# Optimization experiments

Measured on AMD Instinct MI355X. Metric: run time of the kernel, lower is better.

The kernel has to match this reference:

```python
import jax, jax.numpy as jnp
import numpy as np

B, N, L, ND = 512, 4096, 128, 1


def setup_inputs() -> dict:
    key = jax.random.key(0)
    ks = jax.random.split(key, 20)
    g = lambda k, shape, s=0.05: jax.random.normal(k, shape, dtype=jnp.float32) * s
    IN = 3 * L + ND  # MLP input: [mem, mem, delta_t, x]
    inp = {
        "x": jax.random.normal(ks[0], (B, N, ND), jnp.float32),
        "memory": jax.random.normal(ks[1], (N, L), jnp.float32),
        "delta_t": jax.random.normal(ks[2], (B, N, L), jnp.float32),
        "src_w1": g(ks[3], (L, IN)), "src_b1": g(ks[4], (L,)),
        "src_w2": g(ks[5], (L, L)), "src_b2": g(ks[6], (L,)),
        "tar_w1": g(ks[7], (L, IN)), "tar_b1": g(ks[8], (L,)),
        "tar_w2": g(ks[9], (L, L)), "tar_b2": g(ks[10], (L,)),
        "gru_wih": g(ks[11], (3 * L, L)), "gru_whh": g(ks[12], (3 * L, L)),
        "gru_bih": g(ks[13], (3 * L,)), "gru_bhh": g(ks[14], (3 * L,)),
        "source": jax.random.randint(ks[15], (B, 1), 0, N, dtype=jnp.int64),
        "target": jax.random.randint(ks[16], (B, 1), 0, N, dtype=jnp.int64),
    }
    return inp


def _mlp(h, w1, b1, w2, b2):
    return jax.nn.relu(h @ w1.T + b1) @ w2.T + b2


def _gru_cell(inp, h, wih, whh, bih, bhh):
    gi = inp @ wih.T + bih          # [n, 3L]
    gh = h @ whh.T + bhh            # [n, 3L]
    i_r, i_z, i_n = jnp.split(gi, 3, axis=-1)
    h_r, h_z, h_n = jnp.split(gh, 3, axis=-1)
    r = jax.nn.sigmoid(i_r + h_r)
    z = jax.nn.sigmoid(i_z + h_z)
    n = jnp.tanh(i_n + r * h_n)
    return (1.0 - z) * n + z * h


def reference(x, memory, delta_t, src_w1, src_b1, src_w2, src_b2,
              tar_w1, tar_b1, tar_w2, tar_b2,
              gru_wih, gru_whh, gru_bih, gru_bhh, source, target):
    b = x.shape[0]
    bi = jnp.arange(b)
    s = source[:, 0]
    t = target[:, 0]
    src_mem = memory[s]                 # [B, L]
    tar_mem = memory[t]                 # [B, L]
    src_x = x[bi, s, :]                 # [B, ND]
    tar_x = x[bi, t, :]
    src_dt = delta_t[bi, s, :]          # [B, L]
    tar_dt = delta_t[bi, t, :]
    src_in = jnp.concatenate([src_mem, tar_mem, src_dt, src_x], axis=-1)
    tar_in = jnp.concatenate([tar_mem, src_mem, tar_dt, tar_x], axis=-1)
    src_msg = _mlp(src_in, src_w1, src_b1, src_w2, src_b2)
    tar_msg = _mlp(tar_in, tar_w1, tar_b1, tar_w2, tar_b2)

    # unique + scatter_mean == segment-mean over node ids, touching only seen nodes
    ids = jnp.concatenate([s, t], axis=0)                       # [2B]
    msgs = jnp.concatenate([src_msg, tar_msg], axis=0)          # [2B, L]
    n_nodes = memory.shape[0]
    msg_sum = jax.ops.segment_sum(msgs, ids, num_segments=n_nodes)
    cnt = jax.ops.segment_sum(jnp.ones((ids.shape[0],), msgs.dtype), ids,
                              num_segments=n_nodes)
    agg = msg_sum / jnp.maximum(cnt, 1.0)[:, None]              # [N, L]
    new_mem = _gru_cell(agg, memory, gru_wih, gru_whh, gru_bih, gru_bhh)
    seen = (cnt > 0)[:, None]
    return jnp.where(seen, new_mem, memory)
```

## Files before the change

kernel.cpp:

```cpp
#include <hip/hip_runtime.h>
#include <math.h>

#define BB 512
#define NN 4096
#define LL 128
#define IN_DIM 385
#define IN_PAD 388
#define NK4_1 97
#define NK4_2 32
#define EPB 2
#define GPB 4

#define OFF_MSG   0
#define OFF_CNT   (OFF_MSG + NN * LL)
#define OFF_COUNT (OFF_CNT + NN)
#define OFF_LIST  (OFF_COUNT + 4)
#define OFF_W1PS  529416
#define OFF_W1PT  (OFF_W1PS + NK4_1 * LL * 4)
#define OFF_W2PS  (OFF_W1PT + NK4_1 * LL * 4)
#define OFF_W2PT  (OFF_W2PS + NK4_2 * LL * 4)
#define OFF_WIHP  (OFF_W2PT + NK4_2 * LL * 4)
#define OFF_WHHP  (OFF_WIHP + 3 * NK4_2 * LL * 4)

__global__ __launch_bounds__(256) void prep_kernel(
    const float* __restrict__ sw1, const float* __restrict__ tw1,
    const float* __restrict__ sw2, const float* __restrict__ tw2,
    const float* __restrict__ wih, const float* __restrict__ whh,
    float* __restrict__ ws)
{
    const int i = blockIdx.x * 256 + threadIdx.x;
    const int stride = gridDim.x * 256;

    float4* msg4 = (float4*)(ws + OFF_MSG);
    const float4 z4 = make_float4(0.f, 0.f, 0.f, 0.f);
    for (int idx = i; idx < NN * LL / 4; idx += stride)
        msg4[idx] = z4;
    for (int idx = i; idx < NN; idx += stride)
        ws[OFF_CNT + idx] = 0.0f;
    if (i == 0)
        ((int*)ws)[OFF_COUNT] = 0;

    float4* w1ps = (float4*)(ws + OFF_W1PS);
    float4* w1pt = (float4*)(ws + OFF_W1PT);
    for (int idx = i; idx < NK4_1 * LL; idx += stride) {
        const int k4 = idx >> 7, j = idx & 127;
        const int k = k4 * 4;
        float4 a, b;
        a.x = sw1[j * IN_DIM + k];     b.x = tw1[j * IN_DIM + k];
        a.y = (k + 1 < IN_DIM) ? sw1[j * IN_DIM + k + 1] : 0.f;
        b.y = (k + 1 < IN_DIM) ? tw1[j * IN_DIM + k + 1] : 0.f;
        a.z = (k + 2 < IN_DIM) ? sw1[j * IN_DIM + k + 2] : 0.f;
        b.z = (k + 2 < IN_DIM) ? tw1[j * IN_DIM + k + 2] : 0.f;
        a.w = (k + 3 < IN_DIM) ? sw1[j * IN_DIM + k + 3] : 0.f;
        b.w = (k + 3 < IN_DIM) ? tw1[j * IN_DIM + k + 3] : 0.f;
        w1ps[idx] = a; w1pt[idx] = b;
    }
    float4* w2ps = (float4*)(ws + OFF_W2PS);
    float4* w2pt = (float4*)(ws + OFF_W2PT);
    for (int idx = i; idx < NK4_2 * LL; idx += stride) {
        const int k4 = idx >> 7, j = idx & 127;
        const int k = k4 * 4;
        w2ps[idx] = make_float4(sw2[j * LL + k], sw2[j * LL + k + 1],
                                sw2[j * LL + k + 2], sw2[j * LL + k + 3]);
        w2pt[idx] = make_float4(tw2[j * LL + k], tw2[j * LL + k + 1],
                                tw2[j * LL + k + 2], tw2[j * LL + k + 3]);
    }
    float4* wihp = (float4*)(ws + OFF_WIHP);
    float4* whhp = (float4*)(ws + OFF_WHHP);
    for (int idx = i; idx < 3 * NK4_2 * LL; idx += stride) {
        const int j = idx & 127;
        const int gk = idx >> 7;
        const int gate = gk >> 5, k4 = gk & 31;
        const int row = gate * LL + j, k = k4 * 4;
        wihp[idx] = make_float4(wih[row * LL + k], wih[row * LL + k + 1],
                                wih[row * LL + k + 2], wih[row * LL + k + 3]);
        whhp[idx] = make_float4(whh[row * LL + k], whh[row * LL + k + 1],
                                whh[row * LL + k + 2], whh[row * LL + k + 3]);
    }
}

__global__ __launch_bounds__(256) void edge_msg_kernel(
    const float* __restrict__ x,
    const float* __restrict__ memory,
    const float* __restrict__ delta_t,
    const float* __restrict__ sb1, const float* __restrict__ sb2,
    const float* __restrict__ tb1, const float* __restrict__ tb2,
    const int* __restrict__ source, const int* __restrict__ target,
    float* __restrict__ ws, float* __restrict__ out)
{
    const int tid = threadIdx.x;

    if (blockIdx.x >= 512) {
        const int cb = blockIdx.x - 512;
        float4* out4 = (float4*)out;
        const float4* mem4 = (const float4*)memory;
        for (int idx = cb * 256 + tid; idx < NN * LL / 4; idx += 32 * 256)
            out4[idx] = mem4[idx];
        return;
    }

    const int side  = blockIdx.x & 1;
    const int chunk = blockIdx.x >> 1;
    const int g     = tid >> 7;
    const int j     = tid & 127;

    __shared__ float in2[IN_PAD][EPB];
    __shared__ float h1[LL][EPB];
    __shared__ float part1[2][EPB][LL];
    __shared__ float part2[2][EPB][LL];
    __shared__ int   node_sh[EPB];

    const float4* w1p = (const float4*)(ws + (side ? OFF_W1PT : OFF_W1PS));
    const float4* w2p = (const float4*)(ws + (side ? OFF_W2PT : OFF_W2PS));
    const float* b1  = side ? tb1 : sb1;
    const float* b2  = side ? tb2 : sb2;

    #pragma unroll
    for (int e = 0; e < EPB; ++e) {
        const int eg = chunk * EPB + e;
        const int s = source[eg], t = target[eg];
        const int node  = side ? t : s;
        const int other = side ? s : t;
        if (tid == 0) node_sh[e] = node;
        for (int idx = tid; idx < IN_PAD; idx += 256) {
            float v = 0.0f;
            if (idx < LL)           v = memory[node * LL + idx];
            else if (idx < 2 * LL)  v = memory[other * LL + (idx - LL)];
            else if (idx < 3 * LL)  v = delta_t[((size_t)eg * NN + node) * LL + (idx - 2 * LL)];
            else if (idx == 3 * LL) v = x[(size_t)eg * NN + node];
            in2[idx][e] = v;
        }
    }
    __syncthreads();

    {
        const int k40 = g ? 49 : 0;
        const int k41 = g ? NK4_1 : 49;
        float a0 = 0.f, a1 = 0.f;
        #pragma unroll 4
        for (int k4 = k40; k4 < k41; ++k4) {
            const float4 w  = w1p[k4 * LL + j];
            const float4 i0 = *(const float4*)&in2[k4 * 4][0];
            const float4 i1 = *(const float4*)&in2[k4 * 4 + 2][0];
            a0 = fmaf(w.x, i0.x, a0); a1 = fmaf(w.x, i0.y, a1);
            a0 = fmaf(w.y, i0.z, a0); a1 = fmaf(w.y, i0.w, a1);
            a0 = fmaf(w.z, i1.x, a0); a1 = fmaf(w.z, i1.y, a1);
            a0 = fmaf(w.w, i1.z, a0); a1 = fmaf(w.w, i1.w, a1);
        }
        part1[g][0][j] = a0;
        part1[g][1][j] = a1;
    }
    __syncthreads();

    h1[j][g] = fmaxf(part1[0][g][j] + part1[1][g][j] + b1[j], 0.0f);
    __syncthreads();

    {
        const int k40 = g * 16, k41 = k40 + 16;
        float a0 = 0.f, a1 = 0.f;
        #pragma unroll 4
        for (int k4 = k40; k4 < k41; ++k4) {
            const float4 w  = w2p[k4 * LL + j];
            const float4 h0 = *(const float4*)&h1[k4 * 4][0];
            const float4 h2 = *(const float4*)&h1[k4 * 4 + 2][0];
            a0 = fmaf(w.x, h0.x, a0); a1 = fmaf(w.x, h0.y, a1);
            a0 = fmaf(w.y, h0.z, a0); a1 = fmaf(w.y, h0.w, a1);
            a0 = fmaf(w.z, h2.x, a0); a1 = fmaf(w.z, h2.y, a1);
            a0 = fmaf(w.w, h2.z, a0); a1 = fmaf(w.w, h2.w, a1);
        }
        part2[g][0][j] = a0;
        part2[g][1][j] = a1;
    }
    __syncthreads();

    {
        const float m = part2[0][g][j] + part2[1][g][j] + b2[j];
        atomicAdd(ws + OFF_MSG + node_sh[g] * LL + j, m);
    }
    if (tid < EPB) {
        const int node = node_sh[tid];
        const float old = atomicAdd(ws + OFF_CNT + node, 1.0f);
        if (old == 0.0f) {
            const int pos = atomicAdd((int*)ws + OFF_COUNT, 1);
            ((int*)ws)[OFF_LIST + pos] = node;
        }
    }
}

__global__ __launch_bounds__(256) void gru_kernel(
    const float* __restrict__ memory,
    const float* __restrict__ bih, const float* __restrict__ bhh,
    float* __restrict__ ws, float* __restrict__ out)
{
    const int tid = threadIdx.x;
    const int g = tid >> 7, j = tid & 127;
    const int scount = ((const int*)ws)[OFF_COUNT];
    const int base = blockIdx.x * GPB;
    if (base >= scount) return;
    const int nact = min(GPB, scount - base);

    __shared__ float ah[LL][2 * GPB];
    __shared__ float gates[6][GPB][LL];
    __shared__ int   nodes_sh[GPB];

    if (tid < GPB)
        nodes_sh[tid] = (base + tid < scount)
                        ? ((const int*)ws)[OFF_LIST + base + tid] : -1;
    __syncthreads();

    #pragma unroll
    for (int gi = 0; gi < GPB; ++gi) {
        const int node = nodes_sh[gi];
        if (g == 0) {
            float v = 0.0f;
            if (node >= 0) {
                const float c = ws[OFF_CNT + node];
                v = ws[OFF_MSG + node * LL + j] / c;
            }
            ah[j][gi] = v;
        } else {
            ah[j][GPB + gi] = (node >= 0) ? memory[node * LL + j] : 0.0f;
        }
    }
    __syncthreads();

    const float4* wp = (const float4*)(ws + (g ? OFF_WHHP : OFF_WIHP));
    float a0[GPB] = {}, a1[GPB] = {}, a2[GPB] = {};
    #pragma unroll 2
    for (int k4 = 0; k4 < NK4_2; ++k4) {
        const float4 w0 = wp[(0 * NK4_2 + k4) * LL + j];
        const float4 w1 = wp[(1 * NK4_2 + k4) * LL + j];
        const float4 w2 = wp[(2 * NK4_2 + k4) * LL + j];
        const float w0a[4] = {w0.x, w0.y, w0.z, w0.w};
        const float w1a[4] = {w1.x, w1.y, w1.z, w1.w};
        const float w2a[4] = {w2.x, w2.y, w2.z, w2.w};
        #pragma unroll
        for (int c = 0; c < 4; ++c) {
            const float4 v4 = *(const float4*)&ah[k4 * 4 + c][g * GPB];
            const float va[4] = {v4.x, v4.y, v4.z, v4.w};
            #pragma unroll
            for (int gi = 0; gi < GPB; ++gi) {
                a0[gi] = fmaf(w0a[c], va[gi], a0[gi]);
                a1[gi] = fmaf(w1a[c], va[gi], a1[gi]);
                a2[gi] = fmaf(w2a[c], va[gi], a2[gi]);
            }
        }
    }
    #pragma unroll
    for (int gi = 0; gi < GPB; ++gi) {
        gates[g * 3 + 0][gi][j] = a0[gi];
        gates[g * 3 + 1][gi][j] = a1[gi];
        gates[g * 3 + 2][gi][j] = a2[gi];
    }
    __syncthreads();

    const int total = nact * LL;
    for (int o = tid; o < total; o += 256) {
        const int gi = o >> 7, jj = o & 127;
        const int node = nodes_sh[gi];
        const float ir = gates[0][gi][jj] + bih[jj];
        const float iz = gates[1][gi][jj] + bih[LL + jj];
        const float inn = gates[2][gi][jj] + bih[2 * LL + jj];
        const float hr = gates[3][gi][jj] + bhh[jj];
        const float hz = gates[4][gi][jj] + bhh[LL + jj];
        const float hn = gates[5][gi][jj] + bhh[2 * LL + jj];
        const float r = 1.0f / (1.0f + __expf(-(ir + hr)));
        const float z = 1.0f / (1.0f + __expf(-(iz + hz)));
        const float n = tanhf(inn + r * hn);
        const float h = ah[jj][GPB + gi];
        out[node * LL + jj] = (1.0f - z) * n + z * h;
    }
}

extern "C" void kernel_launch(void* const* d_in, const int* in_sizes, int n_in,
                              void* d_out, int out_size, void* d_ws, size_t ws_size,
                              hipStream_t stream) {
    const float* x        = (const float*)d_in[0];
    const float* memory   = (const float*)d_in[1];
    const float* delta_t  = (const float*)d_in[2];
    const float* src_w1   = (const float*)d_in[3];
    const float* src_b1   = (const float*)d_in[4];
    const float* src_w2   = (const float*)d_in[5];
    const float* src_b2   = (const float*)d_in[6];
    const float* tar_w1   = (const float*)d_in[7];
    const float* tar_b1   = (const float*)d_in[8];
    const float* tar_w2   = (const float*)d_in[9];
    const float* tar_b2   = (const float*)d_in[10];
    const float* gru_wih  = (const float*)d_in[11];
    const float* gru_whh  = (const float*)d_in[12];
    const float* gru_bih  = (const float*)d_in[13];
    const float* gru_bhh  = (const float*)d_in[14];
    const int*   source   = (const int*)d_in[15];
    const int*   target   = (const int*)d_in[16];

    float* out = (float*)d_out;
    float* ws  = (float*)d_ws;

    prep_kernel<<<512, 256, 0, stream>>>(
        src_w1, tar_w1, src_w2, tar_w2, gru_wih, gru_whh, ws);

    edge_msg_kernel<<<544, 256, 0, stream>>>(
        x, memory, delta_t, src_b1, src_b2, tar_b1, tar_b2,
        source, target, ws, out);

    gru_kernel<<<1024 / GPB, 256, 0, stream>>>(
        memory, gru_bih, gru_bhh, ws, out);
}
```

Baseline: 37.11 us.

## Read MLP and GRU inputs directly from global memory instead of LDS staging

Both kernels stop staging gathered input rows into shared memory. The message MLP now splits its input by segment (own memory, other memory, delta_t, x) across the two thread groups, and each thread reads wavefront-uniform float4s straight from global memory. The GRU kernel reads the message and memory rows directly and applies the 1/count scale after the matvec, which removes a staging pass and a barrier in each kernel. In exchange every thread issues redundant broadcast global loads that rely on cache hits, and the first layer's work split between the two halves changes slightly.

```diff
diff --git a/kernel.cpp b/kernel.cpp
--- a/kernel.cpp
+++ b/kernel.cpp
@@ -5,7 +5,6 @@
 #define NN 4096
 #define LL 128
 #define IN_DIM 385
-#define IN_PAD 388
 #define NK4_1 97
 #define NK4_2 32
 #define EPB 2
@@ -104,48 +103,78 @@
     const int g     = tid >> 7;
     const int j     = tid & 127;
 
-    __shared__ float in2[IN_PAD][EPB];
+    const int eg0 = chunk * EPB, eg1 = eg0 + 1;
+    const int s0 = source[eg0], t0 = target[eg0];
+    const int s1 = source[eg1], t1 = target[eg1];
+    const int node0  = side ? t0 : s0, other0 = side ? s0 : t0;
+    const int node1  = side ? t1 : s1, other1 = side ? s1 : t1;
+
     __shared__ float h1[LL][EPB];
     __shared__ float part1[2][EPB][LL];
     __shared__ float part2[2][EPB][LL];
-    __shared__ int   node_sh[EPB];
 
     const float4* w1p = (const float4*)(ws + (side ? OFF_W1PT : OFF_W1PS));
     const float4* w2p = (const float4*)(ws + (side ? OFF_W2PT : OFF_W2PS));
     const float* b1  = side ? tb1 : sb1;
     const float* b2  = side ? tb2 : sb2;
 
-    #pragma unroll
-    for (int e = 0; e < EPB; ++e) {
-        const int eg = chunk * EPB + e;
-        const int s = source[eg], t = target[eg];
-        const int node  = side ? t : s;
-        const int other = side ? s : t;
-        if (tid == 0) node_sh[e] = node;
-        for (int idx = tid; idx < IN_PAD; idx += 256) {
-            float v = 0.0f;
-            if (idx < LL)           v = memory[node * LL + idx];
-            else if (idx < 2 * LL)  v = memory[other * LL + (idx - LL)];
-            else if (idx < 3 * LL)  v = delta_t[((size_t)eg * NN + node) * LL + (idx - 2 * LL)];
-            else if (idx == 3 * LL) v = x[(size_t)eg * NN + node];
-            in2[idx][e] = v;
-        }
-    }
-    __syncthreads();
-
     {
-        const int k40 = g ? 49 : 0;
-        const int k41 = g ? NK4_1 : 49;
         float a0 = 0.f, a1 = 0.f;
-        #pragma unroll 4
-        for (int k4 = k40; k4 < k41; ++k4) {
-            const float4 w  = w1p[k4 * LL + j];
-            const float4 i0 = *(const float4*)&in2[k4 * 4][0];
-            const float4 i1 = *(const float4*)&in2[k4 * 4 + 2][0];
-            a0 = fmaf(w.x, i0.x, a0); a1 = fmaf(w.x, i0.y, a1);
-            a0 = fmaf(w.y, i0.z, a0); a1 = fmaf(w.y, i0.w, a1);
-            a0 = fmaf(w.z, i1.x, a0); a1 = fmaf(w.z, i1.y, a1);
-            a0 = fmaf(w.w, i1.z, a0); a1 = fmaf(w.w, i1.w, a1);
+        const float* dA = delta_t + ((size_t)eg0 * NN + node0) * LL;
+        const float* dB = delta_t + ((size_t)eg1 * NN + node1) * LL;
+        if (g == 0) {
+            const float* pA = memory + (size_t)node0 * LL;
+            const float* pB = memory + (size_t)node1 * LL;
+            #pragma unroll 4
+            for (int k4 = 0; k4 < 32; ++k4) {
+                const float4 w  = w1p[k4 * LL + j];
+                const float4 iA = *(const float4*)(pA + 4 * k4);
+                const float4 iB = *(const float4*)(pB + 4 * k4);
+                a0 = fmaf(w.x, iA.x, a0); a1 = fmaf(w.x, iB.x, a1);
+                a0 = fmaf(w.y, iA.y, a0); a1 = fmaf(w.y, iB.y, a1);
+                a0 = fmaf(w.z, iA.z, a0); a1 = fmaf(w.z, iB.z, a1);
+                a0 = fmaf(w.w, iA.w, a0); a1 = fmaf(w.w, iB.w, a1);
+            }
+            #pragma unroll 4
+            for (int k4 = 64; k4 < 80; ++k4) {
+                const float4 w  = w1p[k4 * LL + j];
+                const float4 iA = *(const float4*)(dA + 4 * (k4 - 64));
+                const float4 iB = *(const float4*)(dB + 4 * (k4 - 64));
+                a0 = fmaf(w.x, iA.x, a0); a1 = fmaf(w.x, iB.x, a1);
+                a0 = fmaf(w.y, iA.y, a0); a1 = fmaf(w.y, iB.y, a1);
+                a0 = fmaf(w.z, iA.z, a0); a1 = fmaf(w.z, iB.z, a1);
+                a0 = fmaf(w.w, iA.w, a0); a1 = fmaf(w.w, iB.w, a1);
+            }
+        } else {
+            const float* pA = memory + (size_t)other0 * LL;
+            const float* pB = memory + (size_t)other1 * LL;
+            #pragma unroll 4
+            for (int k4 = 32; k4 < 64; ++k4) {
+                const float4 w  = w1p[k4 * LL + j];
+                const float4 iA = *(const float4*)(pA + 4 * (k4 - 32));
+                const float4 iB = *(const float4*)(pB + 4 * (k4 - 32));
+                a0 = fmaf(w.x, iA.x, a0); a1 = fmaf(w.x, iB.x, a1);
+                a0 = fmaf(w.y, iA.y, a0); a1 = fmaf(w.y, iB.y, a1);
+                a0 = fmaf(w.z, iA.z, a0); a1 = fmaf(w.z, iB.z, a1);
+                a0 = fmaf(w.w, iA.w, a0); a1 = fmaf(w.w, iB.w, a1);
+            }
+            #pragma unroll 4
+            for (int k4 = 80; k4 < 96; ++k4) {
+                const float4 w  = w1p[k4 * LL + j];
+                const float4 iA = *(const float4*)(dA + 4 * (k4 - 64));
+                const float4 iB = *(const float4*)(dB + 4 * (k4 - 64));
+                a0 = fmaf(w.x, iA.x, a0); a1 = fmaf(w.x, iB.x, a1);
+                a0 = fmaf(w.y, iA.y, a0); a1 = fmaf(w.y, iB.y, a1);
+                a0 = fmaf(w.z, iA.z, a0); a1 = fmaf(w.z, iB.z, a1);
+                a0 = fmaf(w.w, iA.w, a0); a1 = fmaf(w.w, iB.w, a1);
+            }
+            {
+                const float4 w = w1p[96 * LL + j];
+                const float xA = x[(size_t)eg0 * NN + node0];
+                const float xB = x[(size_t)eg1 * NN + node1];
+                a0 = fmaf(w.x, xA, a0);
+                a1 = fmaf(w.x, xB, a1);
+            }
         }
         part1[g][0][j] = a0;
         part1[g][1][j] = a1;
@@ -174,11 +203,12 @@
     __syncthreads();
 
     {
+        const int node = g ? node1 : node0;
         const float m = part2[0][g][j] + part2[1][g][j] + b2[j];
-        atomicAdd(ws + OFF_MSG + node_sh[g] * LL + j, m);
+        atomicAdd(ws + OFF_MSG + (size_t)node * LL + j, m);
     }
     if (tid < EPB) {
-        const int node = node_sh[tid];
+        const int node = tid ? node1 : node0;
         const float old = atomicAdd(ws + OFF_CNT + node, 1.0f);
         if (old == 0.0f) {
             const int pos = atomicAdd((int*)ws + OFF_COUNT, 1);
@@ -190,7 +220,8 @@
 __global__ __launch_bounds__(256) void gru_kernel(
     const float* __restrict__ memory,
     const float* __restrict__ bih, const float* __restrict__ bhh,
-    float* __restrict__ ws, float* __restrict__ out)
+    const float* __restrict__ ws,
+    float* __restrict__ out)
 {
     const int tid = threadIdx.x;
     const int g = tid >> 7, j = tid & 127;
@@ -199,30 +230,33 @@
     if (base >= scount) return;
     const int nact = min(GPB, scount - base);
 
-    __shared__ float ah[LL][2 * GPB];
     __shared__ float gates[6][GPB][LL];
     __shared__ int   nodes_sh[GPB];
 
-    if (tid < GPB)
-        nodes_sh[tid] = (base + tid < scount)
-                        ? ((const int*)ws)[OFF_LIST + base + tid] : -1;
-    __syncthreads();
-
+    int nd[GPB];
     #pragma unroll
-    for (int gi = 0; gi < GPB; ++gi) {
-        const int node = nodes_sh[gi];
-        if (g == 0) {
-            float v = 0.0f;
-            if (node >= 0) {
-                const float c = ws[OFF_CNT + node];
-                v = ws[OFF_MSG + node * LL + j] / c;
-            }
-            ah[j][gi] = v;
-        } else {
-            ah[j][GPB + gi] = (node >= 0) ? memory[node * LL + j] : 0.0f;
-        }
-    }
-    __syncthreads();
+    for (int s = 0; s < GPB; ++s)
+        nd[s] = (base + s < scount) ? ((const int*)ws)[OFF_LIST + base + s]
+                                    : ((const int*)ws)[OFF_LIST + base];
+    if (tid < GPB) nodes_sh[tid] = nd[tid];
+
+    const float* op0; const float* op1; const float* op2; const float* op3;
+    float rc0 = 1.f, rc1 = 1.f, rc2 = 1.f, rc3 = 1.f;
+    if (g == 0) {
+        op0 = ws + OFF_MSG + (size_t)nd[0] * LL;
+        op1 = ws + OFF_MSG + (size_t)nd[1] * LL;
+        op2 = ws + OFF_MSG + (size_t)nd[2] * LL;
+        op3 = ws + OFF_MSG + (size_t)nd[3] * LL;
+        rc0 = 1.0f / ws[OFF_CNT + nd[0]];
+        rc1 = 1.0f / ws[OFF_CNT + nd[1]];
+        rc2 = 1.0f / ws[OFF_CNT + nd[2]];
+        rc3 = 1.0f / ws[OFF_CNT + nd[3]];
+    } else {
+        op0 = memory + (size_t)nd[0] * LL;
+        op1 = memory + (size_t)nd[1] * LL;
+        op2 = memory + (size_t)nd[2] * LL;
+        op3 = memory + (size_t)nd[3] * LL;
+    }
 
     const float4* wp = (const float4*)(ws + (g ? OFF_WHHP : OFF_WIHP));
     float a0[GPB] = {}, a1[GPB] = {}, a2[GPB] = {};
@@ -231,44 +265,67 @@
         const float4 w0 = wp[(0 * NK4_2 + k4) * LL + j];
         const float4 w1 = wp[(1 * NK4_2 + k4) * LL + j];
         const float4 w2 = wp[(2 * NK4_2 + k4) * LL + j];
-        const float w0a[4] = {w0.x, w0.y, w0.z, w0.w};
-        const float w1a[4] = {w1.x, w1.y, w1.z, w1.w};
-        const float w2a[4] = {w2.x, w2.y, w2.z, w2.w};
-        #pragma unroll
-        for (int c = 0; c < 4; ++c) {
-            const float4 v4 = *(const float4*)&ah[k4 * 4 + c][g * GPB];
-            const float va[4] = {v4.x, v4.y, v4.z, v4.w};
-            #pragma unroll
-            for (int gi = 0; gi < GPB; ++gi) {
-                a0[gi] = fmaf(w0a[c], va[gi], a0[gi]);
-                a1[gi] = fmaf(w1a[c], va[gi], a1[gi]);
-                a2[gi] = fmaf(w2a[c], va[gi], a2[gi]);
-            }
-        }
+        const float4 v0 = *(const float4*)(op0 + 4 * k4);
+        const float4 v1 = *(const float4*)(op1 + 4 * k4);
+        const float4 v2 = *(const float4*)(op2 + 4 * k4);
+        const float4 v3 = *(const float4*)(op3 + 4 * k4);
+        a0[0] = fmaf(w0.x, v0.x, a0[0]); a0[0] = fmaf(w0.y, v0.y, a0[0]);
+        a0[0] = fmaf(w0.z, v0.z, a0[0]); a0[0] = fmaf(w0.w, v0.w, a0[0]);
+        a1[0] = fmaf(w1.x, v0.x, a1[0]); a1[0] = fmaf(w1.y, v0.y, a1[0]);
+        a1[0] = fmaf(w1.z, v0.z, a1[0]); a1[0] = fmaf(w1.w, v0.w, a1[0]);
+        a2[0] = fmaf(w2.x, v0.x, a2[0]); a2[0] = fmaf(w2.y, v0.y, a2[0]);
+        a2[0] = fmaf(w2.z, v0.z, a2[0]); a2[0] = fmaf(w2.w, v0.w, a2[0]);
+
+        a0[1] = fmaf(w0.x, v1.x, a0[1]); a0[1] = fmaf(w0.y, v1.y, a0[1]);
+        a0[1] = fmaf(w0.z, v1.z, a0[1]); a0[1] = fmaf(w0.w, v1.w, a0[1]);
+        a1[1] = fmaf(w1.x, v1.x, a1[1]); a1[1] = fmaf(w1.y, v1.y, a1[1]);
+        a1[1] = fmaf(w1.z, v1.z, a1[1]); a1[1] = fmaf(w1.w, v1.w, a1[1]);
+        a2[1] = fmaf(w2.x, v1.x, a2[1]); a2[1] = fmaf(w2.y, v1.y, a2[1]);
+        a2[1] = fmaf(w2.z, v1.z, a2[1]); a2[1] = fmaf(w2.w, v1.w, a2[1]);
+
+        a0[2] = fmaf(w0.x, v2.x, a0[2]); a0[2] = fmaf(w0.y, v2.y, a0[2]);
+        a0[2] = fmaf(w0.z, v2.z, a0[2]); a0[2] = fmaf(w0.w, v2.w, a0[2]);
+        a1[2] = fmaf(w1.x, v2.x, a1[2]); a1[2] = fmaf(w1.y, v2.y, a1[2]);
+        a1[2] = fmaf(w1.z, v2.z, a1[2]); a1[2] = fmaf(w1.w, v2.w, a1[2]);
+        a2[2] = fmaf(w2.x, v2.x, a2[2]); a2[2] = fmaf(w2.y, v2.y, a2[2]);
+        a2[2] = fmaf(w2.z, v2.z, a2[2]); a2[2] = fmaf(w2.w, v2.w, a2[2]);
+
+        a0[3] = fmaf(w0.x, v3.x, a0[3]); a0[3] = fmaf(w0.y, v3.y, a0[3]);
+        a0[3] = fmaf(w0.z, v3.z, a0[3]); a0[3] = fmaf(w0.w, v3.w, a0[3]);
+        a1[3] = fmaf(w1.x, v3.x, a1[3]); a1[3] = fmaf(w1.y, v3.y, a1[3]);
+        a1[3] = fmaf(w1.z, v3.z, a1[3]); a1[3] = fmaf(w1.w, v3.w, a1[3]);
+        a2[3] = fmaf(w2.x, v3.x, a2[3]); a2[3] = fmaf(w2.y, v3.y, a2[3]);
+        a2[3] = fmaf(w2.z, v3.z, a2[3]); a2[3] = fmaf(w2.w, v3.w, a2[3]);
+    }
+    if (g == 0) {
+        a0[0] *= rc0; a1[0] *= rc0; a2[0] *= rc0;
+        a0[1] *= rc1; a1[1] *= rc1; a2[1] *= rc1;
+        a0[2] *= rc2; a1[2] *= rc2; a2[2] *= rc2;
+        a0[3] *= rc3; a1[3] *= rc3; a2[3] *= rc3;
     }
     #pragma unroll
-    for (int gi = 0; gi < GPB; ++gi) {
-        gates[g * 3 + 0][gi][j] = a0[gi];
-        gates[g * 3 + 1][gi][j] = a1[gi];
-        gates[g * 3 + 2][gi][j] = a2[gi];
+    for (int s = 0; s < GPB; ++s) {
+        gates[g * 3 + 0][s][j] = a0[s];
+        gates[g * 3 + 1][s][j] = a1[s];
+        gates[g * 3 + 2][s][j] = a2[s];
     }
     __syncthreads();
 
     const int total = nact * LL;
     for (int o = tid; o < total; o += 256) {
-        const int gi = o >> 7, jj = o & 127;
-        const int node = nodes_sh[gi];
-        const float ir = gates[0][gi][jj] + bih[jj];
-        const float iz = gates[1][gi][jj] + bih[LL + jj];
-        const float inn = gates[2][gi][jj] + bih[2 * LL + jj];
-        const float hr = gates[3][gi][jj] + bhh[jj];
-        const float hz = gates[4][gi][jj] + bhh[LL + jj];
-        const float hn = gates[5][gi][jj] + bhh[2 * LL + jj];
+        const int s = o >> 7, jj = o & 127;
+        const int node = nodes_sh[s];
+        const float ir = gates[0][s][jj] + bih[jj];
+        const float iz = gates[1][s][jj] + bih[LL + jj];
+        const float inn = gates[2][s][jj] + bih[2 * LL + jj];
+        const float hr = gates[3][s][jj] + bhh[jj];
+        const float hz = gates[4][s][jj] + bhh[LL + jj];
+        const float hn = gates[5][s][jj] + bhh[2 * LL + jj];
         const float r = 1.0f / (1.0f + __expf(-(ir + hr)));
         const float z = 1.0f / (1.0f + __expf(-(iz + hz)));
         const float n = tanhf(inn + r * hn);
-        const float h = ah[jj][GPB + gi];
-        out[node * LL + jj] = (1.0f - z) * n + z * h;
+        const float h = memory[(size_t)node * LL + jj];
+        out[(size_t)node * LL + jj] = (1.0f - z) * n + z * h;
     }
 }
 
```

Result: faster. 35.68 us (-3.9%).

## Use one edge per block and read MLP/GRU inputs directly from global memory

Applied to the files above, without the earlier changes.

The edge-message kernel now processes one edge per block instead of two, doubling the grid. Each thread reads the memory, delta_t and x rows straight from global memory (warp-uniform broadcast loads) instead of staging the concatenated input in shared memory. The GRU kernel drops to two nodes per block, reads its inputs directly from global memory, and applies the 1/count scaling after the matvec. This removes shared-memory staging and barriers and raises block count, but each weight load is now reused across fewer rows, which increases weight traffic from L2.

```diff
diff --git a/kernel.cpp b/kernel.cpp
--- a/kernel.cpp
+++ b/kernel.cpp
@@ -5,11 +5,9 @@
 #define NN 4096
 #define LL 128
 #define IN_DIM 385
-#define IN_PAD 388
 #define NK4_1 97
 #define NK4_2 32
-#define EPB 2
-#define GPB 4
+#define GPB 2
 
 #define OFF_MSG   0
 #define OFF_CNT   (OFF_MSG + NN * LL)
@@ -90,8 +88,8 @@
 {
     const int tid = threadIdx.x;
 
-    if (blockIdx.x >= 512) {
-        const int cb = blockIdx.x - 512;
+    if (blockIdx.x >= 1024) {
+        const int cb = blockIdx.x - 1024;
         float4* out4 = (float4*)out;
         const float4* mem4 = (const float4*)memory;
         for (int idx = cb * 256 + tid; idx < NN * LL / 4; idx += 32 * 256)
@@ -99,86 +97,92 @@
         return;
     }
 
-    const int side  = blockIdx.x & 1;
-    const int chunk = blockIdx.x >> 1;
-    const int g     = tid >> 7;
-    const int j     = tid & 127;
-
-    __shared__ float in2[IN_PAD][EPB];
-    __shared__ float h1[LL][EPB];
-    __shared__ float part1[2][EPB][LL];
-    __shared__ float part2[2][EPB][LL];
-    __shared__ int   node_sh[EPB];
+    const int side = blockIdx.x & 1;
+    const int eg   = blockIdx.x >> 1;
+    const int g    = tid >> 7;
+    const int j    = tid & 127;
+
+    const int s = source[eg], t = target[eg];
+    const int node  = side ? t : s;
+    const int other = side ? s : t;
+
+    __shared__ float h1[LL];
+    __shared__ float part1[2][LL];
+    __shared__ float part2[2][LL];
 
     const float4* w1p = (const float4*)(ws + (side ? OFF_W1PT : OFF_W1PS));
     const float4* w2p = (const float4*)(ws + (side ? OFF_W2PT : OFF_W2PS));
     const float* b1  = side ? tb1 : sb1;
     const float* b2  = side ? tb2 : sb2;
 
-    #pragma unroll
-    for (int e = 0; e < EPB; ++e) {
-        const int eg = chunk * EPB + e;
-        const int s = source[eg], t = target[eg];
-        const int node  = side ? t : s;
-        const int other = side ? s : t;
-        if (tid == 0) node_sh[e] = node;
-        for (int idx = tid; idx < IN_PAD; idx += 256) {
-            float v = 0.0f;
-            if (idx < LL)           v = memory[node * LL + idx];
-            else if (idx < 2 * LL)  v = memory[other * LL + (idx - LL)];
-            else if (idx < 3 * LL)  v = delta_t[((size_t)eg * NN + node) * LL + (idx - 2 * LL)];
-            else if (idx == 3 * LL) v = x[(size_t)eg * NN + node];
-            in2[idx][e] = v;
-        }
+    {
+        float a0 = 0.f;
+        if (g == 0) {
+            const float* p = memory + (size_t)node * LL;
+            #pragma unroll 4
+            for (int k4 = 0; k4 < 32; ++k4) {
+                const float4 w = w1p[k4 * LL + j];
+                const float4 v = *(const float4*)(p + 4 * k4);
+                a0 = fmaf(w.x, v.x, a0); a0 = fmaf(w.y, v.y, a0);
+                a0 = fmaf(w.z, v.z, a0); a0 = fmaf(w.w, v.w, a0);
+            }
+            const float* q = memory + (size_t)other * LL;
+            #pragma unroll 4
+            for (int k4 = 32; k4 < 48; ++k4) {
+                const float4 w = w1p[k4 * LL + j];
+                const float4 v = *(const float4*)(q + 4 * (k4 - 32));
+                a0 = fmaf(w.x, v.x, a0); a0 = fmaf(w.y, v.y, a0);
+                a0 = fmaf(w.z, v.z, a0); a0 = fmaf(w.w, v.w, a0);
+            }
+        } else {
+            const float* q = memory + (size_t)other * LL;
+            #pragma unroll 4
+            for (int k4 = 48; k4 < 64; ++k4) {
+                const float4 w = w1p[k4 * LL + j];
+                const float4 v = *(const float4*)(q + 4 * (k4 - 32));
+                a0 = fmaf(w.x, v.x, a0); a0 = fmaf(w.y, v.y, a0);
+                a0 = fmaf(w.z, v.z, a0); a0 = fmaf(w.w, v.w, a0);
+            }
+            const float* d = delta_t + ((size_t)eg * NN + node) * LL;
+            #pragma unroll 4
+            for (int k4 = 64; k4 < 96; ++k4) {
+                const float4 w = w1p[k4 * LL + j];
+                const float4 v = *(const float4*)(d + 4 * (k4 - 64));
+                a0 = fmaf(w.x, v.x, a0); a0 = fmaf(w.y, v.y, a0);
+                a0 = fmaf(w.z, v.z, a0); a0 = fmaf(w.w, v.w, a0);
+            }
+            {
+                const float4 w = w1p[96 * LL + j];
+                a0 = fmaf(w.x, x[(size_t)eg * NN + node], a0);
+            }
+        }
+        part1[g][j] = a0;
     }
     __syncthreads();
 
+    if (g == 0)
+        h1[j] = fmaxf(part1[0][j] + part1[1][j] + b1[j], 0.0f);
+    __syncthreads();
+
     {
-        const int k40 = g ? 49 : 0;
-        const int k41 = g ? NK4_1 : 49;
-        float a0 = 0.f, a1 = 0.f;
+        const int k40 = g * 16, k41 = k40 + 16;
+        float a0 = 0.f;
         #pragma unroll 4
         for (int k4 = k40; k4 < k41; ++k4) {
-            const float4 w  = w1p[k4 * LL + j];
-            const float4 i0 = *(const float4*)&in2[k4 * 4][0];
-            const float4 i1 = *(const float4*)&in2[k4 * 4 + 2][0];
-            a0 = fmaf(w.x, i0.x, a0); a1 = fmaf(w.x, i0.y, a1);
-            a0 = fmaf(w.y, i0.z, a0); a1 = fmaf(w.y, i0.w, a1);
-            a0 = fmaf(w.z, i1.x, a0); a1 = fmaf(w.z, i1.y, a1);
-            a0 = fmaf(w.w, i1.z, a0); a1 = fmaf(w.w, i1.w, a1);
-        }
-        part1[g][0][j] = a0;
-        part1[g][1][j] = a1;
+            const float4 w = w2p[k4 * LL + j];
+            const float4 hA = *(const float4*)&h1[k4 * 4];
+            a0 = fmaf(w.x, hA.x, a0); a0 = fmaf(w.y, hA.y, a0);
+            a0 = fmaf(w.z, hA.z, a0); a0 = fmaf(w.w, hA.w, a0);
+        }
+        part2[g][j] = a0;
     }
     __syncthreads();
 
-    h1[j][g] = fmaxf(part1[0][g][j] + part1[1][g][j] + b1[j], 0.0f);
-    __syncthreads();
-
-    {
-        const int k40 = g * 16, k41 = k40 + 16;
-        float a0 = 0.f, a1 = 0.f;
-        #pragma unroll 4
-        for (int k4 = k40; k4 < k41; ++k4) {
-            const float4 w  = w2p[k4 * LL + j];
-            const float4 h0 = *(const float4*)&h1[k4 * 4][0];
-            const float4 h2 = *(const float4*)&h1[k4 * 4 + 2][0];
-            a0 = fmaf(w.x, h0.x, a0); a1 = fmaf(w.x, h0.y, a1);
-            a0 = fmaf(w.y, h0.z, a0); a1 = fmaf(w.y, h0.w, a1);
-            a0 = fmaf(w.z, h2.x, a0); a1 = fmaf(w.z, h2.y, a1);
-            a0 = fmaf(w.w, h2.z, a0); a1 = fmaf(w.w, h2.w, a1);
-        }
-        part2[g][0][j] = a0;
-        part2[g][1][j] = a1;
-    }
-    __syncthreads();
-
-    {
-        const float m = part2[0][g][j] + part2[1][g][j] + b2[j];
-        atomicAdd(ws + OFF_MSG + node_sh[g] * LL + j, m);
-    }
-    if (tid < EPB) {
-        const int node = node_sh[tid];
+    if (g == 0) {
+        const float m = part2[0][j] + part2[1][j] + b2[j];
+        atomicAdd(ws + OFF_MSG + (size_t)node * LL + j, m);
+    }
+    if (tid == 0) {
         const float old = atomicAdd(ws + OFF_CNT + node, 1.0f);
         if (old == 0.0f) {
             const int pos = atomicAdd((int*)ws + OFF_COUNT, 1);
@@ -190,7 +194,7 @@
 __global__ __launch_bounds__(256) void gru_kernel(
     const float* __restrict__ memory,
     const float* __restrict__ bih, const float* __restrict__ bhh,
-    float* __restrict__ ws, float* __restrict__ out)
+    const float* __restrict__ ws, float* __restrict__ out)
 {
     const int tid = threadIdx.x;
     const int g = tid >> 7, j = tid & 127;
@@ -199,30 +203,27 @@
     if (base >= scount) return;
     const int nact = min(GPB, scount - base);
 
-    __shared__ float ah[LL][2 * GPB];
     __shared__ float gates[6][GPB][LL];
     __shared__ int   nodes_sh[GPB];
 
-    if (tid < GPB)
-        nodes_sh[tid] = (base + tid < scount)
-                        ? ((const int*)ws)[OFF_LIST + base + tid] : -1;
-    __syncthreads();
-
+    int nd[GPB];
     #pragma unroll
-    for (int gi = 0; gi < GPB; ++gi) {
-        const int node = nodes_sh[gi];
+    for (int s = 0; s < GPB; ++s)
+        nd[s] = (base + s < scount) ? ((const int*)ws)[OFF_LIST + base + s]
+                                    : ((const int*)ws)[OFF_LIST + base];
+    if (tid < GPB) nodes_sh[tid] = nd[tid];
+
+    const float* op[GPB];
+    float rc[GPB] = {1.f, 1.f};
+    #pragma unroll
+    for (int s = 0; s < GPB; ++s) {
         if (g == 0) {
-            float v = 0.0f;
-            if (node >= 0) {
-                const float c = ws[OFF_CNT + node];
-                v = ws[OFF_MSG + node * LL + j] / c;
-            }
-            ah[j][gi] = v;
+            op[s] = ws + OFF_MSG + (size_t)nd[s] * LL;
+            rc[s] = 1.0f / ws[OFF_CNT + nd[s]];
         } else {
-            ah[j][GPB + gi] = (node >= 0) ? memory[node * LL + j] : 0.0f;
-        }
-    }
-    __syncthreads();
+            op[s] = memory + (size_t)nd[s] * LL;
+        }
+    }
 
     const float4* wp = (const float4*)(ws + (g ? OFF_WHHP : OFF_WIHP));
     float a0[GPB] = {}, a1[GPB] = {}, a2[GPB] = {};
@@ -231,44 +232,40 @@
         const float4 w0 = wp[(0 * NK4_2 + k4) * LL + j];
         const float4 w1 = wp[(1 * NK4_2 + k4) * LL + j];
         const float4 w2 = wp[(2 * NK4_2 + k4) * LL + j];
-        const float w0a[4] = {w0.x, w0.y, w0.z, w0.w};
-        const float w1a[4] = {w1.x, w1.y, w1.z, w1.w};
-        const float w2a[4] = {w2.x, w2.y, w2.z, w2.w};
         #pragma unroll
-        for (int c = 0; c < 4; ++c) {
-            const float4 v4 = *(const float4*)&ah[k4 * 4 + c][g * GPB];
-            const float va[4] = {v4.x, v4.y, v4.z, v4.w};
-            #pragma unroll
-            for (int gi = 0; gi < GPB; ++gi) {
-                a0[gi] = fmaf(w0a[c], va[gi], a0[gi]);
-                a1[gi] = fmaf(w1a[c], va[gi], a1[gi]);
-                a2[gi] = fmaf(w2a[c], va[gi], a2[gi]);
-            }
+        for (int s = 0; s < GPB; ++s) {
+            const float4 v = *(const float4*)(op[s] + 4 * k4);
+            a0[s] = fmaf(w0.x, v.x, a0[s]); a0[s] = fmaf(w0.y, v.y, a0[s]);
+            a0[s] = fmaf(w0.z, v.z, a0[s]); a0[s] = fmaf(w0.w, v.w, a0[s]);
+            a1[s] = fmaf(w1.x, v.x, a1[s]); a1[s] = fmaf(w1.y, v.y, a1[s]);
+            a1[s] = fmaf(w1.z, v.z, a1[s]); a1[s] = fmaf(w1.w, v.w, a1[s]);
+            a2[s] = fmaf(w2.x, v.x, a2[s]); a2[s] = fmaf(w2.y, v.y, a2[s]);
+            a2[s] = fmaf(w2.z, v.z, a2[s]); a2[s] = fmaf(w2.w, v.w, a2[s]);
         }
     }
     #pragma unroll
-    for (int gi = 0; gi < GPB; ++gi) {
-        gates[g * 3 + 0][gi][j] = a0[gi];
-        gates[g * 3 + 1][gi][j] = a1[gi];
-        gates[g * 3 + 2][gi][j] = a2[gi];
+    for (int s = 0; s < GPB; ++s) {
+        gates[g * 3 + 0][s][j] = a0[s] * rc[s];
+        gates[g * 3 + 1][s][j] = a1[s] * rc[s];
+        gates[g * 3 + 2][s][j] = a2[s] * rc[s];
     }
     __syncthreads();
 
     const int total = nact * LL;
     for (int o = tid; o < total; o += 256) {
-        const int gi = o >> 7, jj = o & 127;
-        const int node = nodes_sh[gi];
-        const float ir = gates[0][gi][jj] + bih[jj];
-        const float iz = gates[1][gi][jj] + bih[LL + jj];
-        const float inn = gates[2][gi][jj] + bih[2 * LL + jj];
-        const float hr = gates[3][gi][jj] + bhh[jj];
-        const float hz = gates[4][gi][jj] + bhh[LL + jj];
-        const float hn = gates[5][gi][jj] + bhh[2 * LL + jj];
+        const int s = o >> 7, jj = o & 127;
+        const int node = nodes_sh[s];
+        const float ir = gates[0][s][jj] + bih[jj];
+        const float iz = gates[1][s][jj] + bih[LL + jj];
+        const float inn = gates[2][s][jj] + bih[2 * LL + jj];
+        const float hr = gates[3][s][jj] + bhh[jj];
+        const float hz = gates[4][s][jj] + bhh[LL + jj];
+        const float hn = gates[5][s][jj] + bhh[2 * LL + jj];
         const float r = 1.0f / (1.0f + __expf(-(ir + hr)));
         const float z = 1.0f / (1.0f + __expf(-(iz + hz)));
         const float n = tanhf(inn + r * hn);
-        const float h = ah[jj][GPB + gi];
-        out[node * LL + jj] = (1.0f - z) * n + z * h;
+        const float h = memory[(size_t)node * LL + jj];
+        out[(size_t)node * LL + jj] = (1.0f - z) * n + z * h;
     }
 }
 
@@ -299,7 +296,7 @@
     prep_kernel<<<512, 256, 0, stream>>>(
         src_w1, tar_w1, src_w2, tar_w2, gru_wih, gru_whh, ws);
 
-    edge_msg_kernel<<<544, 256, 0, stream>>>(
+    edge_msg_kernel<<<1056, 256, 0, stream>>>(
         x, memory, delta_t, src_b1, src_b2, tar_b1, tar_b2,
         source, target, ws, out);
 
```

New measurement: 43.45 us. +17.1%, slower.
